# Optimization experiments

Hardware: AMD Instinct MI355X
Metric: run time of the kernel (lower is better)

Reference implementation:

```python
import jax, jax.numpy as jnp
import numpy as np

NX, NH, NY, T = 128, 512, 1, 16384


def setup_inputs() -> dict:
    key = jax.random.key(0)
    ks = jax.random.split(key, 10)
    s = 0.01
    return {
        "x_t": jax.random.normal(ks[0], (T, 1), dtype=jnp.float32),
        "Wf": jax.random.normal(ks[1], (NH, NX), dtype=jnp.float32) * s,
        "Uf": jax.random.normal(ks[2], (NH, NH), dtype=jnp.float32) * s,
        "bf": jnp.zeros((NH,), dtype=jnp.float32),
        "Wi": jax.random.normal(ks[3], (NH, NX), dtype=jnp.float32) * s,
        "Ui": jax.random.normal(ks[4], (NH, NH), dtype=jnp.float32) * s,
        "bi": jnp.zeros((NH,), dtype=jnp.float32),
        "Wo": jax.random.normal(ks[5], (NH, NX), dtype=jnp.float32) * s,
        "Uo": jax.random.normal(ks[6], (NH, NH), dtype=jnp.float32) * s,
        "bo": jnp.zeros((NH,), dtype=jnp.float32),
        "Wc": jax.random.normal(ks[7], (NH, NX), dtype=jnp.float32) * s,
        "Uc": jax.random.normal(ks[8], (NH, NH), dtype=jnp.float32) * s,
        "bc": jnp.zeros((NH,), dtype=jnp.float32),
        "Ahy": jax.random.normal(ks[9], (NY, NH), dtype=jnp.float32) * s,
        "by": jnp.zeros((NY,), dtype=jnp.float32),
    }


def reference(x_t, Wf, Uf, bf, Wi, Ui, bi, Wo, Uo, bo, Wc, Uc, bc, Ahy, by):
    # x_t: (T, 1) univariate series; sliding windows of length Nx feed each step.
    Tlen = x_t.shape[0]
    Nx = Wf.shape[1]
    Nh = Wf.shape[0]
    steps = Tlen - Nx  # number of recurrent steps

    x = x_t[:, 0]  # (T,)
    idx = jnp.arange(steps)[:, None] + jnp.arange(Nx)[None, :]
    Xw = x[idx]  # (steps, Nx) sliding windows

    # Precompute input projections for all steps (batched GEMMs).
    xf = Xw @ Wf.T + bf  # (steps, Nh)
    xi = Xw @ Wi.T + bi
    xo = Xw @ Wo.T + bo
    xc = Xw @ Wc.T + bc

    def step(carry, inp):
        h, c = carry
        xf_t, xi_t, xo_t, xc_t = inp
        f = jax.nn.sigmoid(xf_t + Uf @ h)
        i = jax.nn.sigmoid(xi_t + Ui @ h)
        o = jax.nn.sigmoid(xo_t + Uo @ h)
        g = jnp.tanh(xc_t + Uc @ h)
        c = f * c + i * g
        h = o * jnp.tanh(c)
        mu = Ahy @ h + by  # (Ny,)
        return (h, c), mu

    init = (jnp.zeros((Nh,), x_t.dtype), jnp.zeros((Nh,), x_t.dtype))
    _, mu = jax.lax.scan(step, init, (xf, xi, xo, xc))
    return mu  # (steps, Ny) == (T-Nx, 1), matching torch's stack(...).unsqueeze(1)
```

## Files before the change

kernel.cpp:

```cpp
#include <hip/hip_runtime.h>

#define NHID 512
#define NXW  128
#define TLEN 16384
#define STEPS (TLEN - NXW)
#define G    32
#define B    512
#define RPW  16
#define RSLOTS 8

#define FOR4(M)  M(0) M(1) M(2) M(3)
#define FOR16(M) M(0) M(1) M(2) M(3) M(4) M(5) M(6) M(7) \
                 M(8) M(9) M(10) M(11) M(12) M(13) M(14) M(15)

__device__ __forceinline__ float sigmoid_f(float v) { return 1.f / (1.f + __expf(-v)); }
__device__ __forceinline__ float tanh_f(float v)    { return 1.f - 2.f / (1.f + __expf(2.f * v)); }

__launch_bounds__(B, 2)
__global__ void lstm_persistent(
    const float* x,
    const float* Wf, const float* Uf, const float* bf,
    const float* Wi, const float* Ui, const float* bi,
    const float* Wo, const float* Uo, const float* bo,
    const float* Wc, const float* Uc, const float* bc,
    unsigned long long* ring,
    float* h_hist)
{
    __shared__ float x_win[256];
    __shared__ __align__(16) float h_buf[8][64];
    __shared__ float partials[2][B];

    const int tid = threadIdx.x;
    const int g   = blockIdx.x;
    const int w   = tid >> 6;
    const int l   = tid & 63;
    const int q   = l >> 4;
    const int row = g * RPW + (l & 15);

    const float* Utab[4] = {Uf, Ui, Uo, Uc};
    const float* Wtab[4] = {Wf, Wi, Wo, Wc};
    const float* Btab[4] = {bf, bi, bo, bc};

    const float4* Up = (const float4*)(Utab[q] + (size_t)row * NHID + w * 64);
    #define DECLU(i) float4 u##i = Up[i];
    FOR16(DECLU)
    const float4* Wp = (const float4*)(Wtab[q] + row * NXW + w * 16);
    #define DECLW(i) float4 wv##i = Wp[i];
    FOR4(DECLW)
    #define PIN(r) asm volatile("" : "+v"(r.x), "+v"(r.y), "+v"(r.z), "+v"(r.w));
    #define PINU(i) PIN(u##i)
    FOR16(PINU)
    #define PINW(i) PIN(wv##i)
    FOR4(PINW)

    float bias = 0.f, c_prev = 0.f;
    if (w == 0) bias = Btab[q][row];

    h_buf[w][l] = 0.f;

    for (int t = 0; t < STEPS; ++t) {
        if ((t & 127) == 0) {
            __syncthreads();
            if (tid < 256) {
                int gi = t + tid;
                x_win[tid] = (gi < TLEN) ? x[gi] : 0.f;
            }
            __syncthreads();
        }

        float xacc = 0.f;
        {
            const int xb = (t & 127) + w * 16;
            #define XF(i) xacc += wv##i.x * x_win[xb + 4*i]     \
                                + wv##i.y * x_win[xb + 4*i + 1] \
                                + wv##i.z * x_win[xb + 4*i + 2] \
                                + wv##i.w * x_win[xb + 4*i + 3];
            FOR4(XF)
        }

        if (t > 0) {
            const unsigned long long* src =
                ring + ((size_t)((t - 1) & (RSLOTS - 1)) << 9) + (w * 64 + l);
            const unsigned want = (unsigned)(t - 1);
            unsigned long long vv; int guard = 0;
            do {
                vv = __hip_atomic_load(src, __ATOMIC_RELAXED, __HIP_MEMORY_SCOPE_AGENT);
            } while ((unsigned)(vv >> 32) != want && ++guard < (1 << 20));
            h_buf[w][l] = __uint_as_float((unsigned)vv);
        }

        float acc = xacc;
        const float4* hb4 = (const float4*)h_buf[w];
        #define UF(i) { float4 hv = hb4[i];                       \
                        acc += u##i.x * hv.x + u##i.y * hv.y      \
                             + u##i.z * hv.z + u##i.w * hv.w; }
        FOR16(UF)
        partials[t & 1][(w << 6) | l] = acc;
        __syncthreads();

        if (w == 0) {
            const float* p = partials[t & 1];
            float pre = acc + bias;
            #pragma unroll
            for (int s2 = 1; s2 < 8; ++s2) pre += p[s2 * 64 + l];
            float a = (l < 48) ? sigmoid_f(pre) : tanh_f(pre);
            float ai = __shfl(a, l + 16, 64);
            float ao = __shfl(a, l + 32, 64);
            float ag = __shfl(a, l + 48, 64);
            if (l < 16) {
                float c = a * c_prev + ai * ag;
                c_prev = c;
                float h = ao * tanh_f(c);
                unsigned long long pv =
                    ((unsigned long long)(unsigned)t << 32)
                    | (unsigned long long)__float_as_uint(h);
                __hip_atomic_store(
                    ring + ((size_t)(t & (RSLOTS - 1)) << 9) + row, pv,
                    __ATOMIC_RELAXED, __HIP_MEMORY_SCOPE_AGENT);
                h_hist[(size_t)t * NHID + row] = h;
            }
        }
    }
}

__global__ void mu_kernel(const float* __restrict__ h_hist,
                          const float* __restrict__ Ahy,
                          const float* __restrict__ by,
                          float* __restrict__ outp, int steps)
{
    int wave = threadIdx.x >> 6;
    int lane = threadIdx.x & 63;
    int t = blockIdx.x * 4 + wave;
    if (t >= steps) return;
    const float* h = h_hist + (size_t)t * NHID;
    float p = 0.f;
    #pragma unroll
    for (int e = 0; e < 8; e++)
        p += Ahy[e * 64 + lane] * h[e * 64 + lane];
    #pragma unroll
    for (int off = 32; off; off >>= 1) p += __shfl_down(p, off, 64);
    if (lane == 0) outp[t] = p + by[0];
}

extern "C" void kernel_launch(void* const* d_in, const int* in_sizes, int n_in,
                              void* d_out, int out_size, void* d_ws, size_t ws_size,
                              hipStream_t stream)
{
    const float* x  = (const float*)d_in[0];
    const float* Wf = (const float*)d_in[1];
    const float* Uf = (const float*)d_in[2];
    const float* bf = (const float*)d_in[3];
    const float* Wi = (const float*)d_in[4];
    const float* Ui = (const float*)d_in[5];
    const float* bi = (const float*)d_in[6];
    const float* Wo = (const float*)d_in[7];
    const float* Uo = (const float*)d_in[8];
    const float* bo = (const float*)d_in[9];
    const float* Wc = (const float*)d_in[10];
    const float* Uc = (const float*)d_in[11];
    const float* bc = (const float*)d_in[12];
    const float* Ahy = (const float*)d_in[13];
    const float* by  = (const float*)d_in[14];

    unsigned long long* ring = (unsigned long long*)d_ws;
    float* h_hist = (float*)((char*)d_ws + RSLOTS * NHID * 8);

    lstm_persistent<<<G, B, 0, stream>>>(x, Wf, Uf, bf, Wi, Ui, bi,
                                         Wo, Uo, bo, Wc, Uc, bc, ring, h_hist);
    int muBlocks = (STEPS + 3) / 4;
    mu_kernel<<<muBlocks, 256, 0, stream>>>(h_hist, Ahy, by, (float*)d_out, STEPS);
}
```

Before: 25.61 ms.

## Replace per-step block barrier with LDS flags and readlane broadcast of h

Each wave now keeps its fetched h slice in registers and broadcasts it with readlane, instead of staging it through shared memory. The per-step __syncthreads is replaced by per-wave release flags in LDS that wave 0 spins on. The ring poll issues four outstanding loads, and h_hist writes are moved to a designated wave one step later, off the critical path. The aim is to cut barrier and LDS latency in the serial recurrence. The cost is correctness risk from weaker ordering, since relaxed flag loads and the partials buffer could be overwritten two steps ahead, plus guard-timeout fallbacks.

```diff
diff --git a/kernel.cpp b/kernel.cpp
--- a/kernel.cpp
+++ b/kernel.cpp
@@ -15,6 +15,10 @@
 
 __device__ __forceinline__ float sigmoid_f(float v) { return 1.f / (1.f + __expf(-v)); }
 __device__ __forceinline__ float tanh_f(float v)    { return 1.f - 2.f / (1.f + __expf(2.f * v)); }
+
+__device__ __forceinline__ float bcast(unsigned hbits, int k) {
+    return __uint_as_float(__builtin_amdgcn_readlane(hbits, k));
+}
 
 __launch_bounds__(B, 2)
 __global__ void lstm_persistent(
@@ -27,8 +31,8 @@
     float* h_hist)
 {
     __shared__ float x_win[256];
-    __shared__ __align__(16) float h_buf[8][64];
     __shared__ float partials[2][B];
+    __shared__ int   flags[8];
 
     const int tid = threadIdx.x;
     const int g   = blockIdx.x;
@@ -56,7 +60,10 @@
     float bias = 0.f, c_prev = 0.f;
     if (w == 0) bias = Btab[q][row];
 
-    h_buf[w][l] = 0.f;
+    const bool hist_writer = (w == (g >> 2)) && ((l >> 4) == (g & 3));
+
+    if (l == 0) flags[w] = -1;
+    __syncthreads();
 
     for (int t = 0; t < STEPS; ++t) {
         if ((t & 127) == 0) {
@@ -78,27 +85,66 @@
             FOR4(XF)
         }
 
+        float hval = 0.f;
         if (t > 0) {
             const unsigned long long* src =
                 ring + ((size_t)((t - 1) & (RSLOTS - 1)) << 9) + (w * 64 + l);
             const unsigned want = (unsigned)(t - 1);
-            unsigned long long vv; int guard = 0;
-            do {
-                vv = __hip_atomic_load(src, __ATOMIC_RELAXED, __HIP_MEMORY_SCOPE_AGENT);
-            } while ((unsigned)(vv >> 32) != want && ++guard < (1 << 20));
-            h_buf[w][l] = __uint_as_float((unsigned)vv);
-        }
+            #define RL() __hip_atomic_load(src, __ATOMIC_RELAXED, __HIP_MEMORY_SCOPE_AGENT)
+            unsigned long long vv;
+            unsigned long long p0 = RL(), p1 = RL(), p2 = RL(), p3 = RL();
+            int guard = 0;
+            for (;;) {
+                if ((unsigned)(p0 >> 32) == want) { vv = p0; break; } p0 = RL();
+                if ((unsigned)(p1 >> 32) == want) { vv = p1; break; } p1 = RL();
+                if ((unsigned)(p2 >> 32) == want) { vv = p2; break; } p2 = RL();
+                if ((unsigned)(p3 >> 32) == want) { vv = p3; break; } p3 = RL();
+                if (++guard >= (1 << 14)) {
+                    vv = (unsigned long long)want << 32; break;
+                }
+            }
+            hval = __uint_as_float((unsigned)vv);
+        }
+        asm volatile("" ::: "memory");
 
         float acc = xacc;
-        const float4* hb4 = (const float4*)h_buf[w];
-        #define UF(i) { float4 hv = hb4[i];                       \
-                        acc += u##i.x * hv.x + u##i.y * hv.y      \
-                             + u##i.z * hv.z + u##i.w * hv.w; }
-        FOR16(UF)
-        partials[t & 1][(w << 6) | l] = acc;
-        __syncthreads();
+        {
+            const unsigned hbits = __float_as_uint(hval);
+            #define UB(i) { float h0 = bcast(hbits, 4*i);                    \
+                            float h1 = bcast(hbits, 4*i + 1);                \
+                            float h2 = bcast(hbits, 4*i + 2);                \
+                            float h3 = bcast(hbits, 4*i + 3);                \
+                            acc += u##i.x * h0 + u##i.y * h1                 \
+                                 + u##i.z * h2 + u##i.w * h3; }
+            FOR16(UB)
+        }
+
+        if (w > 0) {
+            partials[t & 1][(w << 6) | l] = acc;
+            if (l == 0)
+                __hip_atomic_store(&flags[w], t, __ATOMIC_RELEASE,
+                                   __HIP_MEMORY_SCOPE_WORKGROUP);
+        }
+
+        if (t > 0 && hist_writer)
+            h_hist[(size_t)(t - 1) * NHID + w * 64 + l] = hval;
 
         if (w == 0) {
+            int gd = 0;
+            for (;;) {
+                int f1 = __hip_atomic_load(&flags[1], __ATOMIC_RELAXED, __HIP_MEMORY_SCOPE_WORKGROUP);
+                int f2 = __hip_atomic_load(&flags[2], __ATOMIC_RELAXED, __HIP_MEMORY_SCOPE_WORKGROUP);
+                int f3 = __hip_atomic_load(&flags[3], __ATOMIC_RELAXED, __HIP_MEMORY_SCOPE_WORKGROUP);
+                int f4 = __hip_atomic_load(&flags[4], __ATOMIC_RELAXED, __HIP_MEMORY_SCOPE_WORKGROUP);
+                int f5 = __hip_atomic_load(&flags[5], __ATOMIC_RELAXED, __HIP_MEMORY_SCOPE_WORKGROUP);
+                int f6 = __hip_atomic_load(&flags[6], __ATOMIC_RELAXED, __HIP_MEMORY_SCOPE_WORKGROUP);
+                int f7 = __hip_atomic_load(&flags[7], __ATOMIC_RELAXED, __HIP_MEMORY_SCOPE_WORKGROUP);
+                if (f1 >= t && f2 >= t && f3 >= t && f4 >= t &&
+                    f5 >= t && f6 >= t && f7 >= t) break;
+                if (++gd >= (1 << 16)) break;
+            }
+            asm volatile("" ::: "memory");
+
             const float* p = partials[t & 1];
             float pre = acc + bias;
             #pragma unroll
@@ -117,7 +163,8 @@
                 __hip_atomic_store(
                     ring + ((size_t)(t & (RSLOTS - 1)) << 9) + row, pv,
                     __ATOMIC_RELAXED, __HIP_MEMORY_SCOPE_AGENT);
-                h_hist[(size_t)t * NHID + row] = h;
+                if (t == STEPS - 1)
+                    h_hist[(size_t)t * NHID + row] = h;
             }
         }
     }
```

Result: slower. 33.11 ms (+29.3%).

## Distribute gate reduction across all waves and offload h history writes to readers

Applied to the files above, without the earlier changes.

The cross-wave reduction of gate partials and the LSTM cell update move off the single wave 0 and are spread across all eight waves. Each wave now reduces two rows with lane shuffles over a padded shared-memory partials array. The global h_hist store is taken off the critical path: one designated block writes the previous step's h from the values it already polled, and only the last step is written directly. The intent is to shorten the serial per-step tail before the ring publish. The cost is extra shuffles and a bit more index logic per thread.

```diff
diff --git a/kernel.cpp b/kernel.cpp
--- a/kernel.cpp
+++ b/kernel.cpp
@@ -28,7 +28,7 @@
 {
     __shared__ float x_win[256];
     __shared__ __align__(16) float h_buf[8][64];
-    __shared__ float partials[2][B];
+    __shared__ float partials[2][8][65];
 
     const int tid = threadIdx.x;
     const int g   = blockIdx.x;
@@ -53,8 +53,15 @@
     #define PINW(i) PIN(wv##i)
     FOR4(PINW)
 
-    float bias = 0.f, c_prev = 0.f;
-    if (w == 0) bias = Btab[q][row];
+    const int td   = l >> 5;
+    const int tq   = (l >> 3) & 3;
+    const int ts   = l & 7;
+    const int tout = tq * 16 + 2 * w + td;
+    const int trow = g * RPW + 2 * w + td;
+    const float tbias = Btab[tq][trow];
+    float c_prev = 0.f;
+
+    const bool hist_writer = (w == (g >> 2)) && ((l >> 4) == (g & 3));
 
     h_buf[w][l] = 0.f;
 
@@ -78,6 +85,7 @@
             FOR4(XF)
         }
 
+        float hval = 0.f;
         if (t > 0) {
             const unsigned long long* src =
                 ring + ((size_t)((t - 1) & (RSLOTS - 1)) << 9) + (w * 64 + l);
@@ -86,7 +94,8 @@
             do {
                 vv = __hip_atomic_load(src, __ATOMIC_RELAXED, __HIP_MEMORY_SCOPE_AGENT);
             } while ((unsigned)(vv >> 32) != want && ++guard < (1 << 20));
-            h_buf[w][l] = __uint_as_float((unsigned)vv);
+            hval = __uint_as_float((unsigned)vv);
+            h_buf[w][l] = hval;
         }
 
         float acc = xacc;
@@ -95,31 +104,37 @@
                         acc += u##i.x * hv.x + u##i.y * hv.y      \
                              + u##i.z * hv.z + u##i.w * hv.w; }
         FOR16(UF)
-        partials[t & 1][(w << 6) | l] = acc;
+        partials[t & 1][w][l] = acc;
+
         __syncthreads();
 
-        if (w == 0) {
-            const float* p = partials[t & 1];
-            float pre = acc + bias;
-            #pragma unroll
-            for (int s2 = 1; s2 < 8; ++s2) pre += p[s2 * 64 + l];
-            float a = (l < 48) ? sigmoid_f(pre) : tanh_f(pre);
-            float ai = __shfl(a, l + 16, 64);
-            float ao = __shfl(a, l + 32, 64);
-            float ag = __shfl(a, l + 48, 64);
-            if (l < 16) {
-                float c = a * c_prev + ai * ag;
-                c_prev = c;
-                float h = ao * tanh_f(c);
-                unsigned long long pv =
-                    ((unsigned long long)(unsigned)t << 32)
-                    | (unsigned long long)__float_as_uint(h);
-                __hip_atomic_store(
-                    ring + ((size_t)(t & (RSLOTS - 1)) << 9) + row, pv,
-                    __ATOMIC_RELAXED, __HIP_MEMORY_SCOPE_AGENT);
-                h_hist[(size_t)t * NHID + row] = h;
-            }
+        float sum = partials[t & 1][ts][tout];
+        sum += __shfl_xor(sum, 1, 64);
+        sum += __shfl_xor(sum, 2, 64);
+        sum += __shfl_xor(sum, 4, 64);
+        sum += tbias;
+        float a = (tq < 3) ? sigmoid_f(sum) : tanh_f(sum);
+        const int base = l & 0x27;
+        float fA = __shfl(a, base,        64);
+        float iA = __shfl(a, base | 0x08, 64);
+        float oA = __shfl(a, base | 0x10, 64);
+        float gA = __shfl(a, base | 0x18, 64);
+        float c  = fA * c_prev + iA * gA;
+        c_prev = c;
+        float h = oA * tanh_f(c);
+        if ((l & 31) == 0) {
+            unsigned long long pv =
+                ((unsigned long long)(unsigned)t << 32)
+                | (unsigned long long)__float_as_uint(h);
+            __hip_atomic_store(
+                ring + ((size_t)(t & (RSLOTS - 1)) << 9) + trow, pv,
+                __ATOMIC_RELAXED, __HIP_MEMORY_SCOPE_AGENT);
+            if (t == STEPS - 1)
+                h_hist[(size_t)t * NHID + trow] = h;
         }
+
+        if (t > 0 && hist_writer)
+            h_hist[(size_t)(t - 1) * NHID + w * 64 + l] = hval;
     }
 }
 
```

Result: slower. 30.11 ms (+17.6%).
